# Optimization experiments

Hardware: AMD Instinct MI355X
Metric: run time of the kernel (lower is better)

The kernel has to match this reference:

```python
import jax, jax.numpy as jnp
from jax import lax
import numpy as np

EPS = 1e-5

def _conv1x1(x, w, b=None):
    # x: [B,C,H,W], w: [O,C]
    y = jnp.einsum('oc,bchw->bohw', w, x)
    if b is not None:
        y = y + b[:, None, None]
    return y

def _bn(x, g, b, m, v):
    scale = g / jnp.sqrt(v + EPS)
    return (x - m[:, None, None]) * scale[:, None, None] + b[:, None, None]

def _conv_bn_silu(x, w, g, b, m, v):
    return jax.nn.silu(_bn(_conv1x1(x, w), g, b, m, v))

def _maxpool(x, k):
    p = k // 2
    return lax.reduce_window(x, -jnp.inf, lax.max, (1, 1, k, k), (1, 1, 1, 1),
                             ((0, 0), (0, 0), (p, p), (p, p)))

def _avgpool(x, k):
    # torch AvgPool2d default count_include_pad=True -> divide by k*k
    p = k // 2
    s = lax.reduce_window(x, 0.0, lax.add, (1, 1, k, k), (1, 1, 1, 1),
                          ((0, 0), (0, 0), (p, p), (p, p)))
    return s / float(k * k)

def setup_inputs() -> dict:
    key = jax.random.key(0)
    ks = jax.random.split(key, 18)
    f32 = jnp.float32
    B, C1, H, W = 8, 512, 64, 64
    c_ = C1 // 2          # 256
    C = c_ * 7            # 1792
    Cq = C // 8           # 224
    C2 = 512
    rn = lambda i, sh, s: jax.random.normal(ks[i], sh, dtype=f32) * s
    return {
        'x': rn(0, (B, C1, H, W), 1.0),
        'cv1_w': rn(1, (c_, C1), 0.05),
        'cv1_g': jax.random.uniform(ks[2], (c_,), dtype=f32),
        'cv1_b': rn(3, (c_,), 0.05),
        'cv1_m': jnp.zeros((c_,), f32),
        'cv1_v': jnp.ones((c_,), f32),
        'q_w': rn(4, (Cq, C), 0.02),
        'q_b': rn(5, (Cq,), 0.02),
        'k_w': rn(6, (Cq, C), 0.02),
        'k_b': rn(7, (Cq,), 0.02),
        'v_w': rn(8, (C, C), 0.02),
        'v_b': rn(9, (C,), 0.02),
        'gamma': rn(10, (1,), 0.5),
        'cv2_w': rn(11, (C2, C), 0.02),
        'cv2_g': jax.random.uniform(ks[12], (C2,), dtype=f32),
        'cv2_b': rn(13, (C2,), 0.05),
        'cv2_m': jnp.zeros((C2,), f32),
        'cv2_v': jnp.ones((C2,), f32),
    }

def _criss_cross(cat, q_w, q_b, k_w, k_b, v_w, v_b, gamma):
    B, C, H, W = cat.shape
    q = _conv1x1(cat, q_w, q_b)   # [B,Cq,H,W]
    k = _conv1x1(cat, k_w, k_b)
    v = _conv1x1(cat, v_w, v_b)   # [B,C,H,W]
    # column (H-axis) energies with -inf diagonal, row (W-axis) energies
    eH = jnp.einsum('bchw,bcgw->bhwg', q, k)        # [B,H,W,H]
    diag = jnp.eye(H, dtype=bool)[:, None, :]       # mask where h == g
    eH = jnp.where(diag, -jnp.inf, eH)
    eW = jnp.einsum('bchw,bchv->bhwv', q, k)        # [B,H,W,W]
    att = jax.nn.softmax(jnp.concatenate([eH, eW], axis=-1), axis=-1)
    attH, attW = att[..., :H], att[..., H:]
    outH = jnp.einsum('bcgw,bhwg->bchw', v, attH)
    outW = jnp.einsum('bchv,bhwv->bchw', v, attW)
    return gamma[0] * (outH + outW) + cat

def reference(x, cv1_w, cv1_g, cv1_b, cv1_m, cv1_v,
              q_w, q_b, k_w, k_b, v_w, v_b, gamma,
              cv2_w, cv2_g, cv2_b, cv2_m, cv2_v):
    x1 = _conv_bn_silu(x, cv1_w, cv1_g, cv1_b, cv1_m, cv1_v)   # [B,256,H,W]
    y1 = _maxpool(x1, 5)
    y2 = _maxpool(y1, 5)
    y3 = _maxpool(y2, 5)
    a1 = _avgpool(x1, 13)
    a2 = _avgpool(x1, 9)
    a3 = _avgpool(x1, 5)
    cat = jnp.concatenate([x1, y1, y2, y3, a1, a2, a3], axis=1)  # [B,1792,H,W]
    att = _criss_cross(cat, q_w, q_b, k_w, k_b, v_w, v_b, gamma)
    return _conv_bn_silu(att, cv2_w, cv2_g, cv2_b, cv2_m, cv2_v)
```

## Files before the change

kernel.cpp:

```cpp
#include <hip/hip_runtime.h>


typedef short bf16x8 __attribute__((ext_vector_type(8)));
typedef float f32x4  __attribute__((ext_vector_type(4)));

#define DEV __device__ __forceinline__

DEV float bf2f(unsigned short u) {
    unsigned int i = ((unsigned int)u) << 16;
    float f; __builtin_memcpy(&f, &i, 4); return f;
}
DEV unsigned short f2bf(float f) {
    unsigned int i; __builtin_memcpy(&i, &f, 4);
    unsigned int r = i + 0x7FFFu + ((i >> 16) & 1u);
    return (unsigned short)(r >> 16);
}
DEV float fsilu(float v) { return v / (1.f + __expf(-v)); }

#define GLL(gsrc, ldst)                                                        \
    __builtin_amdgcn_global_load_lds(                                          \
        (const __attribute__((address_space(1))) unsigned int*)(gsrc),         \
        (__attribute__((address_space(3))) unsigned int*)(ldst), 16, 0, 0)

#define MFMA(a, b, c) __builtin_amdgcn_mfma_f32_16x16x32_bf16((a), (b), (c), 0, 0, 0)

#define SBAR do {                                                              \
    __builtin_amdgcn_sched_barrier(0);                                         \
    __builtin_amdgcn_s_barrier();                                              \
    __builtin_amdgcn_sched_barrier(0); } while (0)
#define LGKM0 do {                                                             \
    asm volatile("s_waitcnt lgkmcnt(0)" ::: "memory");                         \
    __builtin_amdgcn_sched_barrier(0); } while (0)
#define VMC(n) do {                                                            \
    asm volatile("s_waitcnt vmcnt(" #n ")" ::: "memory");                      \
    __builtin_amdgcn_sched_barrier(0); } while (0)

__global__ __launch_bounds__(256) void prep_kernel(
    const float* __restrict__ cv1_w, const float* __restrict__ cv1_g,
    const float* __restrict__ cv1_b, const float* __restrict__ cv1_m,
    const float* __restrict__ cv1_v,
    const float* __restrict__ q_w, const float* __restrict__ q_b,
    const float* __restrict__ k_w, const float* __restrict__ k_b,
    const float* __restrict__ v_b, const float* __restrict__ gamma,
    const float* __restrict__ cv2_w, const float* __restrict__ cv2_g,
    const float* __restrict__ cv2_b, const float* __restrict__ cv2_m,
    const float* __restrict__ cv2_v,
    unsigned short* __restrict__ wb1, unsigned short* __restrict__ wqk,
    unsigned short* __restrict__ wc2,
    float* __restrict__ sc1, float* __restrict__ sh1,
    float* __restrict__ sc2, float* __restrict__ sh2,
    float* __restrict__ qkb, float* __restrict__ zeros)
{
    for (int i = blockIdx.x * 256 + threadIdx.x; i < 917504;
         i += gridDim.x * 256) {
        wc2[i] = f2bf(cv2_w[i]);
        int row = i / 1792;
        int col = i - row * 1792;
        float qv = (row < 224) ? q_w[i]
                   : (row < 448) ? k_w[(row - 224) * 1792 + col] : 0.f;
        wqk[i] = f2bf(qv);
        if (i < 131072) wb1[i] = f2bf(cv1_w[i]);
        if (i < 1792) zeros[i] = 0.f;
        if (i < 512) {
            qkb[i] = (i < 224) ? q_b[i] : (i < 448 ? k_b[i - 224] : 0.f);
            float sc = cv2_g[i] * rsqrtf(cv2_v[i] + 1e-5f);
            float dot = 0.f;
            for (int k = 0; k < 1792; ++k) dot += cv2_w[i * 1792 + k] * v_b[k];
            sc2[i] = sc;
            sh2[i] = cv2_b[i] - cv2_m[i] * sc + sc * gamma[0] * dot;
        }
        if (i < 256) {
            float sc = cv1_g[i] * rsqrtf(cv1_v[i] + 1e-5f);
            sc1[i] = sc; sh1[i] = cv1_b[i] - cv1_m[i] * sc;
        }
    }
}

__global__ __launch_bounds__(256) void transpose_x(
    const float* __restrict__ x, unsigned short* __restrict__ xT)
{
    int bid = blockIdx.x;
    int nt = bid & 63, ct = (bid >> 6) & 7, b = bid >> 9;
    __shared__ float tile[64][65];
    int tid = threadIdx.x;
    int n0 = nt * 64, c0 = ct * 64;
#pragma unroll
    for (int it = 0; it < 16; ++it) {
        int idx = tid + it * 256;
        int r = idx >> 6, cc = idx & 63;
        tile[r][cc] = x[((long)(b * 512 + c0 + r)) * 4096 + n0 + cc];
    }
    __syncthreads();
#pragma unroll
    for (int it = 0; it < 16; ++it) {
        int idx = tid + it * 256;
        int r = idx >> 6, cc = idx & 63;
        xT[((long)(b * 4096 + n0 + r)) * 512 + c0 + cc] = f2bf(tile[cc][r]);
    }
}

__global__ __launch_bounds__(256) void transpose_w(
    const float* __restrict__ w, unsigned short* __restrict__ wT)
{
    int bid = blockIdx.x;
    int tx = bid % 28, ty = bid / 28;
    __shared__ float tile[64][65];
    int tid = threadIdx.x;
#pragma unroll
    for (int it = 0; it < 16; ++it) {
        int idx = tid + it * 256;
        int r = idx >> 6, cc = idx & 63;
        tile[r][cc] = w[((long)(ty * 64 + r)) * 1792 + tx * 64 + cc];
    }
    __syncthreads();
#pragma unroll
    for (int it = 0; it < 16; ++it) {
        int idx = tid + it * 256;
        int r = idx >> 6, cc = idx & 63;
        wT[((long)(tx * 64 + r)) * 1792 + ty * 64 + cc] = f2bf(tile[cc][r]);
    }
}

template <int EPI, bool DUAL>
__global__ __launch_bounds__(512, 2) void gemm256(
    const unsigned short* __restrict__ A, const unsigned short* __restrict__ B,
    const unsigned short* __restrict__ A2, const unsigned short* __restrict__ B2,
    int lda, int ldb, int K1, int K2,
    void* __restrict__ outp, int ldo,
    const float* __restrict__ p0, const float* __restrict__ p1)
{
    __shared__ __align__(16) unsigned short Ash[2][2][8192];
    __shared__ __align__(16) unsigned short Bsh[2][2][8192];
    const int tid = threadIdx.x, lane = tid & 63, wave = tid >> 6;
    const int wm = wave >> 2, wn = wave & 3;
    const long tile_m = (long)blockIdx.x * 256;
    const long tile_n = (long)blockIdx.y * 256;
    const int r0 = tid >> 2;
    const int ke0 = ((tid & 3) * 8) ^ (16 * ((r0 >> 3) & 1));
    const unsigned short* As0 = A + (tile_m + r0) * (long)lda + ke0;
    const unsigned short* As1 = A + (tile_m + r0 + 128) * (long)lda + ke0;
    const unsigned short* Bs0 = B + (tile_n + r0) * (long)ldb + ke0;
    const unsigned short* Bs1 = B + (tile_n + r0 + 128) * (long)ldb + ke0;
    const unsigned short* Cs0 = DUAL ? A2 + (tile_m + r0) * (long)lda + ke0 : As0;
    const unsigned short* Cs1 = DUAL ? A2 + (tile_m + r0 + 128) * (long)lda + ke0 : As1;
    const unsigned short* Ds0 = DUAL ? B2 + (tile_n + r0) * (long)ldb + ke0 : Bs0;
    const unsigned short* Ds1 = DUAL ? B2 + (tile_n + r0 + 128) * (long)ldb + ke0 : Bs1;
    const int dst0 = wave * 512;
    const int dst1 = 4096 + wave * 512;
    const int arow = lane & 15;
    const int kgs = ((lane >> 4) << 3) ^ (16 * ((arow >> 3) & 1));
    f32x4 acc[8][4] = {};
    bf16x8 a[8], b[4];
    const int nt1 = K1 >> 6;
    const int nt = nt1 + (DUAL ? (K2 >> 6) : 0);

#define PA0(t) ((DUAL && (t) >= nt1) ? Cs0 + (long)((t) - nt1) * 64 : As0 + (long)(t) * 64)
#define PA1(t) ((DUAL && (t) >= nt1) ? Cs1 + (long)((t) - nt1) * 64 : As1 + (long)(t) * 64)
#define PB0(t) ((DUAL && (t) >= nt1) ? Ds0 + (long)((t) - nt1) * 64 : Bs0 + (long)(t) * 64)
#define PB1(t) ((DUAL && (t) >= nt1) ? Ds1 + (long)((t) - nt1) * 64 : Bs1 + (long)(t) * 64)
#define STGA(db, kh, t) do {                                                   \
    GLL(PA0(t) + (kh) * 32, &Ash[db][kh][dst0]);                               \
    GLL(PA1(t) + (kh) * 32, &Ash[db][kh][dst1]); } while (0)
#define STGB(db, kh, t) do {                                                   \
    GLL(PB0(t) + (kh) * 32, &Bsh[db][kh][dst0]);                               \
    GLL(PB1(t) + (kh) * 32, &Bsh[db][kh][dst1]); } while (0)
#define LDA8(db, ks) do { _Pragma("unroll")                                    \
    for (int m = 0; m < 8; ++m)                                                \
        a[m] = *(const bf16x8*)&Ash[db][ks][(wm * 128 + m * 16 + arow) * 32 + kgs]; \
    } while (0)
#define LDB1(db, ks, n, slot)                                                  \
    b[slot] = *(const bf16x8*)&Bsh[db][ks][(wn * 64 + (n) * 16 + arow) * 32 + kgs]
#define MMA2(lo) do {                                                          \
    __builtin_amdgcn_s_setprio(1);                                             \
    _Pragma("unroll")                                                          \
    for (int m = 0; m < 8; ++m) {                                              \
        acc[m][lo]     = MFMA(a[m], b[lo],     acc[m][lo]);                    \
        acc[m][lo + 1] = MFMA(a[m], b[lo + 1], acc[m][lo + 1]);                \
    }                                                                          \
    __builtin_amdgcn_s_setprio(0); } while (0)

    STGA(0, 0, 0); STGB(0, 0, 0);
    STGA(0, 1, 0); STGB(0, 1, 0);
    {
        const int t1p = (1 < nt) ? 1 : 0;
        STGA(1, 0, t1p); STGB(1, 0, t1p);
    }
    VMC(8);
    SBAR;

    for (int kt = 0; kt < nt; ++kt) {
        const int db = kt & 1, sb = db ^ 1;
        const int t1c = (kt + 1 < nt) ? kt + 1 : nt - 1;
        const int t2c = (kt + 2 < nt) ? kt + 2 : nt - 1;
        LDA8(db, 0);
        LDB1(db, 0, 0, 0); LDB1(db, 0, 1, 1);
        STGA(sb, 1, t1c);
        SBAR; LGKM0;
        MMA2(0);
        SBAR;
        LDB1(db, 0, 2, 2); LDB1(db, 0, 3, 3);
        STGB(sb, 1, t1c);
        SBAR; LGKM0;
        MMA2(2);
        VMC(8);
        SBAR;
        LDA8(db, 1);
        LDB1(db, 1, 0, 0); LDB1(db, 1, 1, 1);
        STGA(db, 0, t2c);
        SBAR; LGKM0;
        MMA2(0);
        SBAR;
        LDB1(db, 1, 2, 2); LDB1(db, 1, 3, 3);
        STGB(db, 0, t2c);
        SBAR; LGKM0;
        MMA2(2);
        VMC(8);
        SBAR;
    }

    const int rbase = (lane >> 4) << 2;
#pragma unroll
    for (int n = 0; n < 4; ++n) {
        const int gcol = (int)tile_n + wn * 64 + n * 16 + arow;
        const float s0 = p0[gcol];
        const float s1 = (EPI != 1) ? p1[gcol] : 0.f;
#pragma unroll
        for (int m = 0; m < 8; ++m) {
            const long grow0 = tile_m + wm * 128 + m * 16 + rbase;
            if (EPI == 4) {
                const long bb = grow0 >> 12, pix = grow0 & 4095;
                float4 o4;
#pragma unroll
                for (int r = 0; r < 4; ++r) {
                    float v = acc[m][n][r] * s0 + s1;
                    ((float*)&o4)[r] = fsilu(v);
                }
                *(float4*)&((float*)outp)[((bb * 512 + gcol)) * 4096 + pix] = o4;
            } else {
#pragma unroll
                for (int r = 0; r < 4; ++r) {
                    float v = acc[m][n][r];
                    if (EPI != 1) { v = v * s0 + s1; v = fsilu(v); }
                    else          { v += s0; }
                    ((unsigned short*)outp)[(grow0 + r) * ldo + gcol] = f2bf(v);
                }
            }
        }
    }
#undef PA0
#undef PA1
#undef PB0
#undef PB1
#undef STGA
#undef STGB
#undef LDA8
#undef LDB1
#undef MMA2
}

template <int I>
__global__ __launch_bounds__(512) void pool_hk(
    const unsigned short* __restrict__ catT, unsigned short* __restrict__ pool)
{
    constexpr int R = 2 * (I + 1);
    constexpr int K = 2 * R + 1;
    const int b = blockIdx.x >> 6, h = blockIdx.x & 63;
    __shared__ __align__(16) unsigned short x1s[64 * 256];
    const int tid = threadIdx.x, lane = tid & 63, wave = tid >> 6;
    const long nb = (long)b * 4096 + h * 64;
#pragma unroll
    for (int j = 0; j < 4; ++j) {
        int chunk = j * 8 + wave;
        int o = chunk * 1024 + lane * 16;
        int e = o >> 1, w = e >> 8, c = e & 255;
        GLL(catT + (nb + w) * 1792 + c, (char*)x1s + chunk * 1024);
    }
    __syncthreads();
    const int c = tid & 255, wg = tid >> 8;
    const int w0 = wg * 32;
    unsigned short* qm = pool + (long)I * 32768 * 256;
    unsigned short* qs = pool + (long)(I + 3) * 32768 * 256;
    const long obase = ((long)b * 4096 + h) * 256 + c;
    float pre[32];
    {
        float run = -1e30f;
        int ph = (w0 + 2 * R - (K - 1)) % K;
#pragma unroll
        for (int t = 0; t < 32 + K - 1; ++t) {
            int p = w0 + R - (K - 1) + t;
            if (ph == 0) run = -1e30f;
            float v = ((unsigned)p < 64u) ? bf2f(x1s[p * 256 + c]) : -1e30f;
            run = fmaxf(run, v);
            if (t >= K - 1) pre[t - (K - 1)] = run;
            ph = (ph + 1 == K) ? 0 : ph + 1;
        }
    }
    {
        float run = -1e30f;
        int ph = (w0 + 31 + (K - 1)) % K;
#pragma unroll
        for (int t = 0; t < 32 + K - 1; ++t) {
            int s = w0 + 31 - R + (K - 1) - t;
            if (ph == K - 1) run = -1e30f;
            float v = ((unsigned)s < 64u) ? bf2f(x1s[s * 256 + c]) : -1e30f;
            run = fmaxf(run, v);
            if (t >= K - 1) {
                int w = s + R;
                qm[obase + (long)w * 16384] =
                    f2bf(fmaxf(run, pre[31 + (K - 1) - t]));
            }
            ph = (ph == 0) ? K - 1 : ph - 1;
        }
    }
    {
        float s = 0.f;
        int lo0 = (w0 - R >= 0) ? w0 - R : 0;
        int hi0 = (w0 + R <= 63) ? w0 + R : 63;
        for (int d = lo0; d <= hi0; ++d) s += bf2f(x1s[d * 256 + c]);
        for (int ww = 0; ww < 32; ++ww) {
            int w = w0 + ww;
            qs[obase + (long)w * 16384] = f2bf(s);
            if (w + 1 + R <= 63) s += bf2f(x1s[(w + 1 + R) * 256 + c]);
            if (w - R >= 0)      s -= bf2f(x1s[(w - R) * 256 + c]);
        }
    }
}

template <int I>
__global__ __launch_bounds__(256) void pool_v(
    const unsigned short* __restrict__ pool, unsigned short* __restrict__ catT)
{
    constexpr int R = 2 * (I + 1);
    constexpr int K = 2 * R + 1;
    constexpr float SCL = (I == 0) ? (1.f / 25.f)
                        : (I == 1) ? (1.f / 81.f) : (1.f / 169.f);
    constexpr int MAXD = 256 * (I + 1);
    constexpr int SUMD = 1536 - 256 * I;
    const int bid = blockIdx.x;
    const int chh = bid & 1, w = (bid >> 1) & 63, b = bid >> 7;
    const int c0 = chh * 128;
    __shared__ __align__(16) unsigned short mslab[64 * 128];
    __shared__ __align__(16) unsigned short sslab[64 * 128];
    const int tid = threadIdx.x, lane = tid & 63, wave = tid >> 6;
    const long sbase = ((long)b * 4096 + (long)w * 64) * 256 + c0;
    const unsigned short* msrc = pool + (long)I * 32768 * 256 + sbase;
    const unsigned short* ssrc = pool + (long)(I + 3) * 32768 * 256 + sbase;
#pragma unroll
    for (int j = 0; j < 4; ++j) {
        int o = j * 4096 + wave * 1024 + lane * 16;
        int hh = o >> 8, ce = (o & 255) >> 1;
        GLL(msrc + hh * 256 + ce, (char*)mslab + (j * 4096 + wave * 1024));
        GLL(ssrc + hh * 256 + ce, (char*)sslab + (j * 4096 + wave * 1024));
    }
    __syncthreads();
    const int c = tid & 127, hg = tid >> 7;
    const int h0 = hg * 32;
    const long dbase = ((long)b * 4096 + w) * 1792 + c0 + c;
    float pre[32];
    {
        float run = -1e30f;
        int ph = (h0 + 2 * R - (K - 1)) % K;
#pragma unroll
        for (int t = 0; t < 32 + K - 1; ++t) {
            int p = h0 + R - (K - 1) + t;
            if (ph == 0) run = -1e30f;
            float v = ((unsigned)p < 64u) ? bf2f(mslab[p * 128 + c]) : -1e30f;
            run = fmaxf(run, v);
            if (t >= K - 1) pre[t - (K - 1)] = run;
            ph = (ph + 1 == K) ? 0 : ph + 1;
        }
    }
    {
        float run = -1e30f;
        int ph = (h0 + 31 + (K - 1)) % K;
#pragma unroll
        for (int t = 0; t < 32 + K - 1; ++t) {
            int s = h0 + 31 - R + (K - 1) - t;
            if (ph == K - 1) run = -1e30f;
            float v = ((unsigned)s < 64u) ? bf2f(mslab[s * 128 + c]) : -1e30f;
            run = fmaxf(run, v);
            if (t >= K - 1) {
                int h = s + R;
                catT[dbase + MAXD + (long)h * (64 * 1792)] =
                    f2bf(fmaxf(run, pre[31 + (K - 1) - t]));
            }
            ph = (ph == 0) ? K - 1 : ph - 1;
        }
    }
    {
        float s = 0.f;
        int lo0 = (h0 - R >= 0) ? h0 - R : 0;
        int hi0 = (h0 + R <= 63) ? h0 + R : 63;
        for (int d = lo0; d <= hi0; ++d) s += bf2f(sslab[d * 128 + c]);
        for (int hh = 0; hh < 32; ++hh) {
            int h = h0 + hh;
            catT[dbase + SUMD + (long)h * (64 * 1792)] = f2bf(s * SCL);
            if (h + 1 + R <= 63) s += bf2f(sslab[(h + 1 + R) * 128 + c]);
            if (h - R >= 0)      s -= bf2f(sslab[(h - R) * 128 + c]);
        }
    }
}

__global__ __launch_bounds__(256) void scores_h(
    const unsigned short* __restrict__ qk, float* __restrict__ attHlog)
{
    const int b = blockIdx.x >> 6, w = blockIdx.x & 63;
    __shared__ __align__(16) unsigned short Qs[64 * 232];
    __shared__ __align__(16) unsigned short Ks[64 * 232];
    const int tid = threadIdx.x, lane = tid & 63, wave = tid >> 6;
#pragma unroll
    for (int j = 0; j < 14; ++j) {
        int idx = tid + j * 256;
        int s = idx >= 1792;
        int id2 = idx - s * 1792;
        int row = id2 / 28, cb = id2 - row * 28;
        bf16x8 v = *(const bf16x8*)(qk + ((long)b * 4096 + row * 64 + w) * 512 +
                                    s * 224 + cb * 8);
        *(bf16x8*)((s ? Ks : Qs) + row * 232 + cb * 8) = v;
    }
    __syncthreads();
    const int m0 = wave * 16, arow = lane & 15, kc = (lane >> 4) << 3;
    f32x4 acc[4] = {};
#pragma unroll
    for (int ks = 0; ks < 7; ++ks) {
        bf16x8 af = *(const bf16x8*)(Qs + (m0 + arow) * 232 + ks * 32 + kc);
#pragma unroll
        for (int nf = 0; nf < 4; ++nf) {
            bf16x8 bv = *(const bf16x8*)(Ks + (nf * 16 + arow) * 232 + ks * 32 + kc);
            acc[nf] = MFMA(af, bv, acc[nf]);
        }
    }
    const int rb = (lane >> 4) << 2;
#pragma unroll
    for (int nf = 0; nf < 4; ++nf) {
        int g = nf * 16 + arow;
#pragma unroll
        for (int r = 0; r < 4; ++r) {
            int h = m0 + rb + r;
            float v = acc[nf][r];
            if (g == h) v = -1e30f;
            attHlog[((long)(b * 64 + h) * 64 + w) * 64 + g] = v;
        }
    }
}

__global__ __launch_bounds__(256) void scores_w_softmax(
    const unsigned short* __restrict__ qk, const float* __restrict__ attHlog,
    unsigned short* __restrict__ att)
{
    const int b = blockIdx.x >> 6, h = blockIdx.x & 63;
    __shared__ __align__(16) unsigned short Qs[64 * 232];
    __shared__ __align__(16) unsigned short Ks[64 * 232];
    __shared__ float ews[64 * 65];
    const int tid = threadIdx.x, lane = tid & 63, wave = tid >> 6;
    const long nbase = (long)b * 4096 + h * 64;
#pragma unroll
    for (int j = 0; j < 14; ++j) {
        int idx = tid + j * 256;
        int s = idx >= 1792;
        int id2 = idx - s * 1792;
        int row = id2 / 28, cb = id2 - row * 28;
        bf16x8 v = *(const bf16x8*)(qk + (nbase + row) * 512 + s * 224 + cb * 8);
        *(bf16x8*)((s ? Ks : Qs) + row * 232 + cb * 8) = v;
    }
    __syncthreads();
    const int m0 = wave * 16, arow = lane & 15, kc = (lane >> 4) << 3;
    f32x4 acc[4] = {};
#pragma unroll
    for (int ks = 0; ks < 7; ++ks) {
        bf16x8 af = *(const bf16x8*)(Qs + (m0 + arow) * 232 + ks * 32 + kc);
#pragma unroll
        for (int nf = 0; nf < 4; ++nf) {
            bf16x8 bv = *(const bf16x8*)(Ks + (nf * 16 + arow) * 232 + ks * 32 + kc);
            acc[nf] = MFMA(af, bv, acc[nf]);
        }
    }
    const int rb = (lane >> 4) << 2;
#pragma unroll
    for (int nf = 0; nf < 4; ++nf)
#pragma unroll
        for (int r = 0; r < 4; ++r)
            ews[(m0 + rb + r) * 65 + nf * 16 + arow] = acc[nf][r];
    __syncthreads();
    const int wl = tid >> 2, p = tid & 3;
    float eh[16], ew[16];
    const float* hrow = attHlog + ((long)(b * 64 + h) * 64 + wl) * 64 + p * 16;
#pragma unroll
    for (int j = 0; j < 16; ++j) eh[j] = hrow[j];
#pragma unroll
    for (int j = 0; j < 16; ++j) ew[j] = ews[wl * 65 + p * 16 + j];
    float mx = -1e30f;
#pragma unroll
    for (int j = 0; j < 16; ++j) { mx = fmaxf(mx, eh[j]); mx = fmaxf(mx, ew[j]); }
    mx = fmaxf(mx, __shfl_xor(mx, 1));
    mx = fmaxf(mx, __shfl_xor(mx, 2));
    float sm = 0.f;
#pragma unroll
    for (int j = 0; j < 16; ++j) {
        eh[j] = __expf(eh[j] - mx); sm += eh[j];
        ew[j] = __expf(ew[j] - mx); sm += ew[j];
    }
    sm += __shfl_xor(sm, 1);
    sm += __shfl_xor(sm, 2);
    float inv = 1.f / sm;
    unsigned short* orow = att + ((long)(b * 64 + h) * 64 + wl) * 128;
#pragma unroll
    for (int j = 0; j < 16; ++j) orow[p * 16 + j] = f2bf(eh[j] * inv);
#pragma unroll
    for (int j = 0; j < 16; ++j) orow[64 + p * 16 + j] = f2bf(ew[j] * inv);
}

template <int MODE>
__global__ __launch_bounds__(256) void apply_att(
    const unsigned short* __restrict__ att, const unsigned short* __restrict__ vsrc,
    unsigned short* __restrict__ mixed, const float* __restrict__ gamma)
{
    const int ch = blockIdx.x & 3;
    const int i  = (blockIdx.x >> 2) & 63;
    const int b  = blockIdx.x >> 8;
    const int c0 = ch * 448;
    __shared__ __align__(16) unsigned short As[64 * 72];
    __shared__ __align__(16) unsigned short Vs[64 * 448];
    const int tid = threadIdx.x, lane = tid & 63, wave = tid >> 6;
#pragma unroll
    for (int j = 0; j < 2; ++j) {
        int idx = tid + j * 256;
        int hh = idx >> 3, cb = idx & 7;
        long pos = (MODE == 0) ? ((long)(b * 64 + hh) * 64 + i)
                               : ((long)(b * 64 + i) * 64 + hh);
        bf16x8 v = *(const bf16x8*)(att + pos * 128 + MODE * 64 + cb * 8);
        *(bf16x8*)(As + hh * 72 + cb * 8) = v;
    }
#pragma unroll
    for (int j = 0; j < 14; ++j) {
        int idx = tid + j * 256;
        int g = idx / 56, cb = idx - g * 56;
        long n = (MODE == 0) ? ((long)b * 4096 + g * 64 + i)
                             : ((long)b * 4096 + i * 64 + g);
        bf16x8 v = *(const bf16x8*)(vsrc + n * 1792 + c0 + cb * 8);
        int sw = (g >> 3) & 7;
        *(bf16x8*)(Vs + g * 448 + ((cb ^ sw) << 3)) = v;
    }
    __syncthreads();
    const int arow = lane & 15, kc8 = (lane >> 4) << 3;
    const int rb = (lane >> 4) << 2;
    f32x4 acc[4][7] = {};
#pragma unroll
    for (int ks = 0; ks < 2; ++ks) {
        const int k0 = ks * 32;
        bf16x8 af[4];
#pragma unroll
        for (int m = 0; m < 4; ++m)
            af[m] = *(const bf16x8*)(As + (m * 16 + arow) * 72 + k0 + kc8);
        const int g0 = k0 + kc8;
        const int sw = (g0 >> 3) & 7;
#pragma unroll
        for (int nf = 0; nf < 7; ++nf) {
            int cl = wave * 112 + nf * 16 + arow;
            int cb = cl >> 3, clo = cl & 7;
            const unsigned short* pp = Vs + g0 * 448 + ((cb ^ sw) << 3) + clo;
            bf16x8 bv;
#pragma unroll
            for (int j = 0; j < 8; ++j) bv[j] = (short)pp[j * 448];
#pragma unroll
            for (int m = 0; m < 4; ++m)
                acc[m][nf] = MFMA(af[m], bv, acc[m][nf]);
        }
    }
    const float gam = gamma[0];
#pragma unroll
    for (int nf = 0; nf < 7; ++nf) {
        const int c = c0 + wave * 112 + nf * 16 + arow;
#pragma unroll
        for (int m = 0; m < 4; ++m) {
#pragma unroll
            for (int r = 0; r < 4; ++r) {
                const int rl = m * 16 + rb + r;
                long n = (MODE == 0) ? ((long)b * 4096 + rl * 64 + i)
                                     : ((long)b * 4096 + i * 64 + rl);
                long idx2 = n * 1792 + c;
                if (MODE == 0) {
                    mixed[idx2] = f2bf(acc[m][nf][r]);
                } else {
                    float pv = bf2f(mixed[idx2]);
                    mixed[idx2] = f2bf(gam * (acc[m][nf][r] + pv));
                }
            }
        }
    }
}

extern "C" void kernel_launch(void* const* d_in, const int* in_sizes, int n_in,
                              void* d_out, int out_size, void* d_ws, size_t ws_size,
                              hipStream_t stream)
{
    const float* x     = (const float*)d_in[0];
    const float* cv1_w = (const float*)d_in[1];
    const float* cv1_g = (const float*)d_in[2];
    const float* cv1_b = (const float*)d_in[3];
    const float* cv1_m = (const float*)d_in[4];
    const float* cv1_v = (const float*)d_in[5];
    const float* q_w   = (const float*)d_in[6];
    const float* q_b   = (const float*)d_in[7];
    const float* k_w   = (const float*)d_in[8];
    const float* k_b   = (const float*)d_in[9];
    const float* v_w   = (const float*)d_in[10];
    const float* v_b   = (const float*)d_in[11];
    const float* gamma = (const float*)d_in[12];
    const float* cv2_w = (const float*)d_in[13];
    const float* cv2_g = (const float*)d_in[14];
    const float* cv2_b = (const float*)d_in[15];
    const float* cv2_m = (const float*)d_in[16];
    const float* cv2_v = (const float*)d_in[17];

    char* ws = (char*)d_ws;
    unsigned short* wb1  = (unsigned short*)(ws + 0);
    unsigned short* wqk  = (unsigned short*)(ws + 262144);
    unsigned short* wc2  = (unsigned short*)(ws + 2097152);
    unsigned short* w2g  = (unsigned short*)(ws + 3932160);
    float* sc1           = (float*)(ws + 5767168);
    float* sh1           = (float*)(ws + 5775360);
    float* sc2           = (float*)(ws + 5783552);
    float* sh2           = (float*)(ws + 5791744);
    float* qkb           = (float*)(ws + 5799936);
    float* zeros         = (float*)(ws + 5808128);
    unsigned short* catT = (unsigned short*)(ws + 6291456);
    const long C_OFF = 123731968;
    unsigned short* xT    = (unsigned short*)(ws + C_OFF);
    unsigned short* wvT   = (unsigned short*)(ws + C_OFF + 33554432);
    unsigned short* poolb = (unsigned short*)(ws + C_OFF);
    unsigned short* mixed = (unsigned short*)(ws + C_OFF);
    unsigned short* qk    = (unsigned short*)d_out;
    float* attHlog        = (float*)((char*)d_out + 33554432);
    unsigned short* attb  = (unsigned short*)((char*)d_out + 41943040);

    prep_kernel<<<1024, 256, 0, stream>>>(
        cv1_w, cv1_g, cv1_b, cv1_m, cv1_v, q_w, q_b, k_w, k_b, v_b, gamma,
        cv2_w, cv2_g, cv2_b, cv2_m, cv2_v,
        wb1, wqk, wc2, sc1, sh1, sc2, sh2, qkb, zeros);

    transpose_x<<<4096, 256, 0, stream>>>(x, xT);
    transpose_w<<<784, 256, 0, stream>>>(v_w, wvT);

    gemm256<1, false><<<dim3(2, 7), 512, 0, stream>>>(
        wc2, wvT, wc2, wvT, 1792, 1792, 1792, 0, w2g, 1792, zeros, nullptr);

    gemm256<0, false><<<dim3(128, 1), 512, 0, stream>>>(
        xT, wb1, xT, wb1, 512, 512, 512, 0, catT, 1792, sc1, sh1);

    pool_hk<0><<<512, 512, 0, stream>>>(catT, poolb);
    pool_hk<1><<<512, 512, 0, stream>>>(catT, poolb);
    pool_hk<2><<<512, 512, 0, stream>>>(catT, poolb);
    pool_v<0><<<1024, 256, 0, stream>>>(poolb, catT);
    pool_v<1><<<1024, 256, 0, stream>>>(poolb, catT);
    pool_v<2><<<1024, 256, 0, stream>>>(poolb, catT);

    gemm256<1, false><<<dim3(128, 2), 512, 0, stream>>>(
        catT, wqk, catT, wqk, 1792, 1792, 1792, 0, qk, 512, qkb, nullptr);

    scores_h<<<512, 256, 0, stream>>>(qk, attHlog);
    scores_w_softmax<<<512, 256, 0, stream>>>(qk, attHlog, attb);

    apply_att<0><<<2048, 256, 0, stream>>>(attb, catT, mixed, gamma);
    apply_att<1><<<2048, 256, 0, stream>>>(attb, catT, mixed, gamma);

    gemm256<4, true><<<dim3(128, 2), 512, 0, stream>>>(
        mixed, w2g, catT, wc2, 1792, 1792, 1792, 1792, d_out, 0, sc2, sh2);
}
```

Baseline: 634.3 us.

## Parallelize cv2 shift dot products and relax GEMM vmcnt waits to deepen pipelining

The per-channel cv2_w·v_b dot product used to run serially in 512 threads of prep_kernel, with 1792 iterations each. It moves to a dedicated kernel that uses one block per channel and a shared-memory tree reduction, so a few long-running threads no longer hold up the prep kernel. Separately, the GEMM main loop now waits for vmcnt(4) once per iteration instead of vmcnt(8) twice, plus a full drain before the epilogue. This lets more global-to-LDS loads stay in flight while the MFMAs run. The looser wait counts risk a race if the in-flight accounting is wrong.

```diff
diff --git a/kernel.cpp b/kernel.cpp
--- a/kernel.cpp
+++ b/kernel.cpp
@@ -41,14 +41,10 @@
     const float* __restrict__ cv1_v,
     const float* __restrict__ q_w, const float* __restrict__ q_b,
     const float* __restrict__ k_w, const float* __restrict__ k_b,
-    const float* __restrict__ v_b, const float* __restrict__ gamma,
-    const float* __restrict__ cv2_w, const float* __restrict__ cv2_g,
-    const float* __restrict__ cv2_b, const float* __restrict__ cv2_m,
-    const float* __restrict__ cv2_v,
+    const float* __restrict__ cv2_w,
     unsigned short* __restrict__ wb1, unsigned short* __restrict__ wqk,
     unsigned short* __restrict__ wc2,
     float* __restrict__ sc1, float* __restrict__ sh1,
-    float* __restrict__ sc2, float* __restrict__ sh2,
     float* __restrict__ qkb, float* __restrict__ zeros)
 {
     for (int i = blockIdx.x * 256 + threadIdx.x; i < 917504;
@@ -61,18 +57,36 @@
         wqk[i] = f2bf(qv);
         if (i < 131072) wb1[i] = f2bf(cv1_w[i]);
         if (i < 1792) zeros[i] = 0.f;
-        if (i < 512) {
-            qkb[i] = (i < 224) ? q_b[i] : (i < 448 ? k_b[i - 224] : 0.f);
-            float sc = cv2_g[i] * rsqrtf(cv2_v[i] + 1e-5f);
-            float dot = 0.f;
-            for (int k = 0; k < 1792; ++k) dot += cv2_w[i * 1792 + k] * v_b[k];
-            sc2[i] = sc;
-            sh2[i] = cv2_b[i] - cv2_m[i] * sc + sc * gamma[0] * dot;
-        }
+        if (i < 512) qkb[i] = (i < 224) ? q_b[i] : (i < 448 ? k_b[i - 224] : 0.f);
         if (i < 256) {
             float sc = cv1_g[i] * rsqrtf(cv1_v[i] + 1e-5f);
             sc1[i] = sc; sh1[i] = cv1_b[i] - cv1_m[i] * sc;
         }
+    }
+}
+
+__global__ __launch_bounds__(256) void sh2_kernel(
+    const float* __restrict__ cv2_w, const float* __restrict__ cv2_g,
+    const float* __restrict__ cv2_b, const float* __restrict__ cv2_m,
+    const float* __restrict__ cv2_v, const float* __restrict__ v_b,
+    const float* __restrict__ gamma,
+    float* __restrict__ sc2, float* __restrict__ sh2)
+{
+    const int i = blockIdx.x, tid = threadIdx.x;
+    __shared__ float red[256];
+    float s = 0.f;
+    for (int k = tid; k < 1792; k += 256) s += cv2_w[i * 1792 + k] * v_b[k];
+    red[tid] = s;
+    __syncthreads();
+#pragma unroll
+    for (int off = 128; off > 0; off >>= 1) {
+        if (tid < off) red[tid] += red[tid + off];
+        __syncthreads();
+    }
+    if (tid == 0) {
+        float sc = cv2_g[i] * rsqrtf(cv2_v[i] + 1e-5f);
+        sc2[i] = sc;
+        sh2[i] = cv2_b[i] - cv2_m[i] * sc + sc * gamma[0] * red[0];
     }
 }
 
@@ -185,7 +199,7 @@
         const int t1p = (1 < nt) ? 1 : 0;
         STGA(1, 0, t1p); STGB(1, 0, t1p);
     }
-    VMC(8);
+    VMC(4);
     SBAR;
 
     for (int kt = 0; kt < nt; ++kt) {
@@ -202,7 +216,6 @@
         STGB(sb, 1, t1c);
         SBAR; LGKM0;
         MMA2(2);
-        VMC(8);
         SBAR;
         LDA8(db, 1);
         LDB1(db, 1, 0, 0); LDB1(db, 1, 1, 1);
@@ -214,9 +227,10 @@
         STGB(db, 0, t2c);
         SBAR; LGKM0;
         MMA2(2);
-        VMC(8);
+        VMC(4);
         SBAR;
     }
+    VMC(0);
 
     const int rbase = (lane >> 4) << 2;
 #pragma unroll
@@ -635,9 +649,11 @@
     unsigned short* attb  = (unsigned short*)((char*)d_out + 41943040);
 
     prep_kernel<<<1024, 256, 0, stream>>>(
-        cv1_w, cv1_g, cv1_b, cv1_m, cv1_v, q_w, q_b, k_w, k_b, v_b, gamma,
-        cv2_w, cv2_g, cv2_b, cv2_m, cv2_v,
-        wb1, wqk, wc2, sc1, sh1, sc2, sh2, qkb, zeros);
+        cv1_w, cv1_g, cv1_b, cv1_m, cv1_v, q_w, q_b, k_w, k_b, cv2_w,
+        wb1, wqk, wc2, sc1, sh1, qkb, zeros);
+
+    sh2_kernel<<<512, 256, 0, stream>>>(
+        cv2_w, cv2_g, cv2_b, cv2_m, cv2_v, v_b, gamma, sc2, sh2);
 
     transpose_x<<<4096, 256, 0, stream>>>(x, xT);
     transpose_w<<<784, 256, 0, stream>>>(v_w, wvT);
```

Result: faster. 587.6 us (-7.4%).
